# Kernel tuning notes

Measured on AMD Instinct MI355X. Metric: run time of the kernel, lower is better.

## Reference

```python
import jax, jax.numpy as jnp
import numpy as np

N_NODES = 50000
N_EDGES = 800000
HID = 256
OUT = 128
NEG_SLOPE = 0.2


def gat_layer(x, src, dst, W_src, W_dst, a_src_vec, a_dst_vec, bias, n_nodes):
    # Dense projections (PyG lin_src / lin_dst for tuple in_channels)
    h_src = x @ W_src              # [N, C]
    h_dst = x @ W_dst              # [N, C]
    # Per-node attention logits (att_src/att_dst dot products)
    a_src = h_src @ a_src_vec      # [N]
    a_dst = h_dst @ a_dst_vec      # [N]
    # Edge logits + LeakyReLU
    e = jax.nn.leaky_relu(a_src[src] + a_dst[dst], NEG_SLOPE)  # [E]
    # Segment softmax over incoming edges of each dst node
    m = jax.ops.segment_max(e, dst, num_segments=n_nodes)      # [N]
    m = jnp.where(jnp.isfinite(m), m, 0.0)                      # empty segments
    ex = jnp.exp(e - m[dst])                                    # [E]
    s = jax.ops.segment_sum(ex, dst, num_segments=n_nodes)     # [N]
    alpha = ex / (s[dst] + 1e-16)                               # [E]
    # Attention-weighted message aggregation (scatter-add to dst)
    msg = alpha[:, None] * h_src[src]                           # [E, C]
    out = jax.ops.segment_sum(msg, dst, num_segments=n_nodes)  # [N, C]
    return out + bias


def setup_inputs() -> dict:
    key = jax.random.key(0)
    ks = jax.random.split(key, 12)
    x = jax.random.normal(ks[0], (N_NODES, HID), dtype=jnp.float32)
    edge_index = jax.random.randint(ks[1], (2, N_EDGES), 0, N_NODES, dtype=jnp.int64)
    sc1 = 1.0 / np.sqrt(HID)
    sc2 = 1.0 / np.sqrt(HID)
    return {
        "x": x,
        "edge_index": edge_index,
        "W1_src": jax.random.normal(ks[2], (HID, HID), dtype=jnp.float32) * sc1,
        "W1_dst": jax.random.normal(ks[3], (HID, HID), dtype=jnp.float32) * sc1,
        "att1_src": jax.random.normal(ks[4], (HID,), dtype=jnp.float32) * sc1,
        "att1_dst": jax.random.normal(ks[5], (HID,), dtype=jnp.float32) * sc1,
        "b1": jnp.zeros((HID,), dtype=jnp.float32),
        "W2_src": jax.random.normal(ks[6], (HID, OUT), dtype=jnp.float32) * sc2,
        "W2_dst": jax.random.normal(ks[7], (HID, OUT), dtype=jnp.float32) * sc2,
        "att2_src": jax.random.normal(ks[8], (OUT,), dtype=jnp.float32) * (1.0 / np.sqrt(OUT)),
        "att2_dst": jax.random.normal(ks[9], (OUT,), dtype=jnp.float32) * (1.0 / np.sqrt(OUT)),
        "b2": jnp.zeros((OUT,), dtype=jnp.float32),
    }


def reference(x, edge_index, W1_src, W1_dst, att1_src, att1_dst, b1,
              W2_src, W2_dst, att2_src, att2_dst, b2):
    src, dst = edge_index[0], edge_index[1]
    h = gat_layer(x, src, dst, W1_src, W1_dst, att1_src, att1_dst, b1, N_NODES)
    h = jax.nn.relu(h)
    out = gat_layer(h, src, dst, W2_src, W2_dst, att2_src, att2_dst, b2, N_NODES)
    return out
```

## Files before the change

kernel.cpp:

```cpp
#include <hip/hip_runtime.h>
#include <math.h>

#define N_NODES 50000
#define N_EDGES 800000
#define HID 256
#define OUT_C 128
#define NEG_SLOPE 0.2f
#define SCAN_NB ((N_NODES + 255) / 256)

typedef __attribute__((ext_vector_type(8))) short bf16x8;
typedef __attribute__((ext_vector_type(4))) float f32x4;
typedef _Float16 half_t;
typedef __attribute__((ext_vector_type(4))) _Float16 half4;
typedef __attribute__((ext_vector_type(2))) _Float16 half2t;

__device__ inline unsigned short bf16_rne(float x) {
    unsigned u = __float_as_uint(x);
    return (unsigned short)((u + 0x7fffu + ((u >> 16) & 1u)) >> 16);
}


__global__ __launch_bounds__(256) void hist_rank_kernel(
    const int* __restrict__ dst, int* __restrict__ counts, int* __restrict__ rank) {
    int e = blockIdx.x * 256 + threadIdx.x;
    if (e < N_EDGES) rank[e] = atomicAdd(&counts[dst[e]], 1);
}

__global__ __launch_bounds__(256) void block_scan_kernel(
    const int* __restrict__ counts, int* __restrict__ excl,
    int* __restrict__ blockSums, int n) {
    __shared__ int waveSums[4];
    int i = blockIdx.x * 256 + threadIdx.x;
    int lane = threadIdx.x & 63;
    int wv = threadIdx.x >> 6;
    int c = (i < n) ? counts[i] : 0;
    int v = c;
    #pragma unroll
    for (int off = 1; off < 64; off <<= 1) {
        int t = __shfl_up(v, off);
        if (lane >= off) v += t;
    }
    if (lane == 63) waveSums[wv] = v;
    __syncthreads();
    int waveOff = 0;
    #pragma unroll
    for (int w = 0; w < 4; w++)
        if (w < wv) waveOff += waveSums[w];
    if (i < n) excl[i] = waveOff + v - c;
    if (threadIdx.x == 255) blockSums[blockIdx.x] = waveOff + v;
}

__global__ __launch_bounds__(256) void add_offsets_kernel(
    int* __restrict__ excl, const int* __restrict__ blockSums, int n) {
    __shared__ int lds[4];
    int tid = threadIdx.x;
    int partial = 0;
    for (int j = tid; j < (int)blockIdx.x; j += 256) partial += blockSums[j];
    #pragma unroll
    for (int off = 32; off > 0; off >>= 1) partial += __shfl_down(partial, off);
    if ((tid & 63) == 0) lds[tid >> 6] = partial;
    __syncthreads();
    int prefix = lds[0] + lds[1] + lds[2] + lds[3];
    int i = blockIdx.x * 256 + tid;
    if (i < n) excl[i] += prefix;
    if (i == 0) excl[n] = N_EDGES;
}


__global__ __launch_bounds__(256) void edge_weight_kernel(
    const int* __restrict__ src, const int* __restrict__ dst,
    const int* __restrict__ offsets, const int* __restrict__ rank,
    const float* __restrict__ a_src, const float* __restrict__ a_dst,
    int2* __restrict__ ew) {
    int e = blockIdx.x * 256 + threadIdx.x;
    if (e >= N_EDGES) return;
    int s = src[e], d = dst[e];
    float l = a_src[s] + a_dst[d];
    l = fmaxf(l, l * NEG_SLOPE);
    float w = __expf(l);
    ew[offsets[d] + rank[e]] = make_int2(s, __float_as_int(w));
}


__global__ __launch_bounds__(64) void compute_v_all_kernel(
    const float* __restrict__ W1s, const float* __restrict__ att1s,
    const float* __restrict__ W1d, const float* __restrict__ att1d,
    const float* __restrict__ W2s, const float* __restrict__ att2s,
    const float* __restrict__ W2d, const float* __restrict__ att2d,
    float* __restrict__ v1s, float* __restrict__ v1d,
    float* __restrict__ v2s, float* __restrict__ v2d) {
    int k = blockIdx.x;
    int lane = threadIdx.x;
    const float* W; const float* att; float* v; int cout;
    switch (blockIdx.y) {
        case 0: W = W1s; att = att1s; v = v1s; cout = HID; break;
        case 1: W = W1d; att = att1d; v = v1d; cout = HID; break;
        case 2: W = W2s; att = att2s; v = v2s; cout = OUT_C; break;
        default: W = W2d; att = att2d; v = v2d; cout = OUT_C; break;
    }
    float sum = 0.f;
    for (int j = lane; j < cout; j += 64)
        sum += W[k * cout + j] * att[j];
    #pragma unroll
    for (int off = 32; off > 0; off >>= 1)
        sum += __shfl_down(sum, off);
    if (lane == 0) v[k] = sum;
}


#define PACK1_T (8 * 17 * 64)
#define PACK2_T (8 * 9 * 64)

__global__ __launch_bounds__(256) void pack_all_kernel(
    const float* __restrict__ W1, const float* __restrict__ v1s, const float* __restrict__ v1d,
    const float* __restrict__ W2, const float* __restrict__ v2s, const float* __restrict__ v2d,
    unsigned short* __restrict__ hi1, unsigned short* __restrict__ lo1,
    unsigned short* __restrict__ hi2, unsigned short* __restrict__ lo2) {
    int t = blockIdx.x * 256 + threadIdx.x;
    const float *W, *vs, *vd; unsigned short *hi, *lo; int cout, NTL, tt;
    if (t < PACK1_T)            { tt = t;           W = W1; vs = v1s; vd = v1d; hi = hi1; lo = lo1; cout = HID;  NTL = 17; }
    else if (t < PACK1_T + PACK2_T) { tt = t - PACK1_T; W = W2; vs = v2s; vd = v2d; hi = hi2; lo = lo2; cout = OUT_C; NTL = 9; }
    else return;
    int lane = tt & 63;
    int tile = (tt >> 6) % NTL;
    int ks = tt / (64 * NTL);
    int m = lane & 15;
    int kbase = ks * 32 + (lane >> 4) * 8;
    #pragma unroll
    for (int j = 0; j < 8; j++) {
        float val;
        if (tile < NTL - 1) val = W[(kbase + j) * cout + tile * 16 + m];
        else val = (m == 0) ? vs[kbase + j] : (m == 1) ? vd[kbase + j] : 0.f;
        unsigned short h = bf16_rne(val);
        hi[tt * 8 + j] = h;
        lo[tt * 8 + j] = bf16_rne(val - __uint_as_float((unsigned)h << 16));
    }
}


template <int COUT, int NT, bool WRITE_A>
__device__ __forceinline__ void gemm_body(
    const float* __restrict__ A, const unsigned short* __restrict__ Bhi,
    const unsigned short* __restrict__ Blo, half_t* __restrict__ H,
    float* __restrict__ a_s, float* __restrict__ a_d, int M, int tile0) {
    const int NTL = COUT / 16 + 1;
    int wave = threadIdx.x >> 6, lane = threadIdx.x & 63;
    int m = lane & 15, quad = lane >> 4;
    int row0 = blockIdx.x * 128 + wave * 32;
    f32x4 acc[2][NT];
    #pragma unroll
    for (int rg = 0; rg < 2; rg++)
        #pragma unroll
        for (int nt = 0; nt < NT; nt++)
            acc[rg][nt] = (f32x4){0.f, 0.f, 0.f, 0.f};

    const float* arow[2];
    #pragma unroll
    for (int rg = 0; rg < 2; rg++) {
        int r = row0 + rg * 16 + m;
        if (r >= M) r = M - 1;
        arow[rg] = A + (size_t)r * HID;
    }

    for (int ks = 0; ks < 8; ks++) {
        bf16x8 ah[2], al[2];
        #pragma unroll
        for (int rg = 0; rg < 2; rg++) {
            const float* ap = arow[rg] + ks * 32 + quad * 8;
            float4 v0 = *(const float4*)ap;
            float4 v1 = *(const float4*)(ap + 4);
            float av[8] = {v0.x, v0.y, v0.z, v0.w, v1.x, v1.y, v1.z, v1.w};
            #pragma unroll
            for (int j = 0; j < 8; j++) {
                unsigned short h = bf16_rne(av[j]);
                float hf = __uint_as_float((unsigned)h << 16);
                ah[rg][j] = (short)h;
                al[rg][j] = (short)bf16_rne(av[j] - hf);
            }
        }
        #pragma unroll
        for (int nt = 0; nt < NT; nt++) {
            int tile = (WRITE_A && nt == NT - 1) ? (COUT / 16) : (tile0 + nt);
            size_t fbase = ((size_t)(ks * NTL + tile) * 64 + lane) * 8;
            bf16x8 bh = *(const bf16x8*)(Bhi + fbase);
            bf16x8 bl = *(const bf16x8*)(Blo + fbase);
            acc[0][nt] = __builtin_amdgcn_mfma_f32_16x16x32_bf16(ah[0], bh, acc[0][nt], 0, 0, 0);
            acc[1][nt] = __builtin_amdgcn_mfma_f32_16x16x32_bf16(ah[1], bh, acc[1][nt], 0, 0, 0);
            acc[0][nt] = __builtin_amdgcn_mfma_f32_16x16x32_bf16(ah[0], bl, acc[0][nt], 0, 0, 0);
            acc[1][nt] = __builtin_amdgcn_mfma_f32_16x16x32_bf16(ah[1], bl, acc[1][nt], 0, 0, 0);
            acc[0][nt] = __builtin_amdgcn_mfma_f32_16x16x32_bf16(al[0], bh, acc[0][nt], 0, 0, 0);
            acc[1][nt] = __builtin_amdgcn_mfma_f32_16x16x32_bf16(al[1], bh, acc[1][nt], 0, 0, 0);
        }
    }
    const int NW = WRITE_A ? NT - 1 : NT;
    #pragma unroll
    for (int rg = 0; rg < 2; rg++)
        #pragma unroll
        for (int nt = 0; nt < NW; nt++)
            #pragma unroll
            for (int r = 0; r < 4; r++) {
                int row = row0 + rg * 16 + quad * 4 + r;
                if (row < M)
                    H[(size_t)row * COUT + (tile0 + nt) * 16 + m] = (half_t)acc[rg][nt][r];
            }
    if (WRITE_A) {
        #pragma unroll
        for (int rg = 0; rg < 2; rg++)
            #pragma unroll
            for (int r = 0; r < 4; r++) {
                int row = row0 + rg * 16 + quad * 4 + r;
                if (row < M) {
                    if (m == 0) a_s[row] = acc[rg][NT - 1][r];
                    else if (m == 1) a_d[row] = acc[rg][NT - 1][r];
                }
            }
    }
}

template <int COUT>
__global__ __launch_bounds__(256) void mfma_gemm_a_kernel(
    const float* __restrict__ A, const unsigned short* __restrict__ Bhi,
    const unsigned short* __restrict__ Blo, half_t* __restrict__ H,
    float* __restrict__ a_s, float* __restrict__ a_d, int M) {
    if (blockIdx.y == 0)
        gemm_body<COUT, 9, true>(A, Bhi, Blo, H, a_s, a_d, M, 0);
    else
        gemm_body<COUT, 8, false>(A, Bhi, Blo, H, a_s, a_d, M, 8);
}


template <int C, bool RELU>
__global__ __launch_bounds__(256) void fused_aggregate_kernel(
    const int* __restrict__ offsets, const int2* __restrict__ ew,
    const half_t* __restrict__ h, const float* __restrict__ bias,
    float* __restrict__ out) {
    constexpr int CH = 8;
    int node = (int)((blockIdx.x * 256u + threadIdx.x) >> 6);
    int lane = threadIdx.x & 63;
    if (node >= N_NODES) return;
    int beg = offsets[node], end = offsets[node + 1];
    float s = 0.f;

    if (C == 256) {
        float4 acc = make_float4(0.f, 0.f, 0.f, 0.f);
        for (int base = beg; base < end; base += CH) {
            int cnt = end - base; if (cnt > CH) cnt = CH;
            int2 e[CH];
            #pragma unroll
            for (int j = 0; j < CH; j++)
                e[j] = ew[(j < cnt) ? base + j : base];
            half4 hv[CH];
            #pragma unroll
            for (int j = 0; j < CH; j++)
                hv[j] = *(const half4*)(h + ((unsigned)e[j].x * C + lane * 4));
            #pragma unroll
            for (int j = 0; j < CH; j++) {
                float w = (j < cnt) ? __int_as_float(e[j].y) : 0.f;
                s += w;
                acc.x += w * (float)hv[j][0]; acc.y += w * (float)hv[j][1];
                acc.z += w * (float)hv[j][2]; acc.w += w * (float)hv[j][3];
            }
        }
        float inv = 1.f / (s + 1e-16f);
        float4 bv = *(const float4*)(bias + lane * 4);
        acc.x = acc.x * inv + bv.x; acc.y = acc.y * inv + bv.y;
        acc.z = acc.z * inv + bv.z; acc.w = acc.w * inv + bv.w;
        if (RELU) {
            acc.x = fmaxf(acc.x, 0.f); acc.y = fmaxf(acc.y, 0.f);
            acc.z = fmaxf(acc.z, 0.f); acc.w = fmaxf(acc.w, 0.f);
        }
        *(float4*)(out + (size_t)node * C + lane * 4) = acc;
    } else {
        float2 acc = make_float2(0.f, 0.f);
        for (int base = beg; base < end; base += CH) {
            int cnt = end - base; if (cnt > CH) cnt = CH;
            int2 e[CH];
            #pragma unroll
            for (int j = 0; j < CH; j++)
                e[j] = ew[(j < cnt) ? base + j : base];
            half2t hv[CH];
            #pragma unroll
            for (int j = 0; j < CH; j++)
                hv[j] = *(const half2t*)(h + ((unsigned)e[j].x * C + lane * 2));
            #pragma unroll
            for (int j = 0; j < CH; j++) {
                float w = (j < cnt) ? __int_as_float(e[j].y) : 0.f;
                s += w;
                acc.x += w * (float)hv[j][0]; acc.y += w * (float)hv[j][1];
            }
        }
        float inv = 1.f / (s + 1e-16f);
        float2 bv = *(const float2*)(bias + lane * 2);
        acc.x = acc.x * inv + bv.x; acc.y = acc.y * inv + bv.y;
        if (RELU) { acc.x = fmaxf(acc.x, 0.f); acc.y = fmaxf(acc.y, 0.f); }
        *(float2*)(out + (size_t)node * C + lane * 2) = acc;
    }
}

extern "C" void kernel_launch(void* const* d_in, const int* in_sizes, int n_in,
                              void* d_out, int out_size, void* d_ws, size_t ws_size,
                              hipStream_t stream) {
    const float* x     = (const float*)d_in[0];
    const int*   edge  = (const int*)d_in[1];
    const int*   src   = edge;
    const int*   dst   = edge + N_EDGES;
    const float* W1s   = (const float*)d_in[2];
    const float* W1d   = (const float*)d_in[3];
    const float* att1s = (const float*)d_in[4];
    const float* att1d = (const float*)d_in[5];
    const float* b1    = (const float*)d_in[6];
    const float* W2s   = (const float*)d_in[7];
    const float* W2d   = (const float*)d_in[8];
    const float* att2s = (const float*)d_in[9];
    const float* att2d = (const float*)d_in[10];
    const float* b2    = (const float*)d_in[11];
    float* out = (float*)d_out;

    float* ws    = (float*)d_ws;
    half_t* h1   = (half_t*)ws;
    int2* ew     = (int2*)(ws + (size_t)N_NODES * HID / 2);
    float* act2  = ws + (size_t)N_NODES * HID;
    float* a_s   = act2 + (size_t)N_NODES * HID;
    float* a_d   = a_s + N_NODES;
    float* vbuf  = a_d + N_NODES;
    int* ibase      = (int*)(vbuf + 4 * HID);
    int* rank       = ibase;
    int* counts     = rank + N_EDGES;
    int* offsets    = counts + N_NODES;
    int* blockSums  = offsets + N_NODES + 1;
    unsigned short* wp1h = (unsigned short*)(((uintptr_t)(blockSums + SCAN_NB) + 15) & ~(uintptr_t)15);
    unsigned short* wp1l = wp1h + PACK1_T * 8;
    unsigned short* wp2h = wp1l + PACK1_T * 8;
    unsigned short* wp2l = wp2h + PACK2_T * 8;
    float* v1s = vbuf, *v1d = vbuf + HID, *v2s = vbuf + 2 * HID, *v2d = vbuf + 3 * HID;
    half_t* h2 = h1;

    const int edgeBlocks = (N_EDGES + 255) / 256;
    const int waveBlocksN = (N_NODES + 3) / 4;
    const int gemmBlocks = (N_NODES + 127) / 128;

    hipMemsetAsync(counts, 0, N_NODES * sizeof(int), stream);
    hist_rank_kernel<<<edgeBlocks, 256, 0, stream>>>(dst, counts, rank);
    block_scan_kernel<<<SCAN_NB, 256, 0, stream>>>(counts, offsets, blockSums, N_NODES);
    add_offsets_kernel<<<SCAN_NB, 256, 0, stream>>>(offsets, blockSums, N_NODES);

    compute_v_all_kernel<<<dim3(HID, 4), 64, 0, stream>>>(
        W1s, att1s, W1d, att1d, W2s, att2s, W2d, att2d, v1s, v1d, v2s, v2d);
    pack_all_kernel<<<(PACK1_T + PACK2_T + 255) / 256, 256, 0, stream>>>(
        W1s, v1s, v1d, W2s, v2s, v2d, wp1h, wp1l, wp2h, wp2l);

    mfma_gemm_a_kernel<HID><<<dim3(gemmBlocks, 2), 256, 0, stream>>>(
        x, wp1h, wp1l, h1, a_s, a_d, N_NODES);
    edge_weight_kernel<<<edgeBlocks, 256, 0, stream>>>(
        src, dst, offsets, rank, a_s, a_d, ew);
    fused_aggregate_kernel<HID, true><<<waveBlocksN, 256, 0, stream>>>(
        offsets, ew, h1, b1, act2);

    mfma_gemm_a_kernel<OUT_C><<<dim3(gemmBlocks, 1), 256, 0, stream>>>(
        act2, wp2h, wp2l, h2, a_s, a_d, N_NODES);
    edge_weight_kernel<<<edgeBlocks, 256, 0, stream>>>(
        src, dst, offsets, rank, a_s, a_d, ew);
    fused_aggregate_kernel<OUT_C, false><<<waveBlocksN, 256, 0, stream>>>(
        offsets, ew, h2, b2, out);
}
```

Baseline: 361.9 us.

## Pack multiple nodes per wave in aggregation with 16-byte gathers and shuffled edge loads

The aggregation kernel now assigns 2 nodes (C=256) or 4 nodes (C=128) per 64-lane wave, so each lane handles 8 channels and gathers a 16-byte half8 vector per edge. Edge records are loaded cooperatively, one per lane, and broadcast with width-limited shuffles instead of every lane reloading all of them. The chunk size rises to 16 edges. The goal is fewer wasted lanes and wider memory transactions for the low-degree (about 16 edges) gather, in exchange for more registers and shuffle overhead.

```diff
diff --git a/kernel.cpp b/kernel.cpp
--- a/kernel.cpp
+++ b/kernel.cpp
@@ -11,8 +11,7 @@
 typedef __attribute__((ext_vector_type(8))) short bf16x8;
 typedef __attribute__((ext_vector_type(4))) float f32x4;
 typedef _Float16 half_t;
-typedef __attribute__((ext_vector_type(4))) _Float16 half4;
-typedef __attribute__((ext_vector_type(2))) _Float16 half2t;
+typedef __attribute__((ext_vector_type(8))) _Float16 half8;
 
 __device__ inline unsigned short bf16_rne(float x) {
     unsigned u = __float_as_uint(x);
@@ -234,67 +233,62 @@
     const int* __restrict__ offsets, const int2* __restrict__ ew,
     const half_t* __restrict__ h, const float* __restrict__ bias,
     float* __restrict__ out) {
-    constexpr int CH = 8;
-    int node = (int)((blockIdx.x * 256u + threadIdx.x) >> 6);
+    constexpr int CH = 16;
+    constexpr int G = (C == 256) ? 32 : 16;
+    constexpr int NPW = 64 / G;
+    int wid = blockIdx.x * 4 + (threadIdx.x >> 6);
     int lane = threadIdx.x & 63;
+    int sub = lane / G;
+    int gl = lane & (G - 1);
+    int node = wid * NPW + sub;
     if (node >= N_NODES) return;
     int beg = offsets[node], end = offsets[node + 1];
-    float s = 0.f;
-
-    if (C == 256) {
-        float4 acc = make_float4(0.f, 0.f, 0.f, 0.f);
-        for (int base = beg; base < end; base += CH) {
-            int cnt = end - base; if (cnt > CH) cnt = CH;
-            int2 e[CH];
+    float ssum = 0.f;
+    float acc[8];
+    #pragma unroll
+    for (int k = 0; k < 8; k++) acc[k] = 0.f;
+    unsigned c0 = (unsigned)gl * 8u;
+
+    for (int base = beg; base < end; base += CH) {
+        int cnt = end - base; if (cnt > CH) cnt = CH;
+        int li = gl & (CH - 1);
+        int eidx = base + ((li < cnt) ? li : 0);
+        int2 ev = ew[eidx];
+        int idxs[CH]; float w[CH];
+        #pragma unroll
+        for (int j = 0; j < CH; j++) {
+            idxs[j] = __shfl(ev.x, j, G);
+            float wv = __int_as_float(__shfl(ev.y, j, G));
+            w[j] = (j < cnt) ? wv : 0.f;
+        }
+        half8 hv[CH];
+        #pragma unroll
+        for (int j = 0; j < CH; j++)
+            hv[j] = *(const half8*)(h + ((size_t)(unsigned)idxs[j] * C + c0));
+        #pragma unroll
+        for (int j = 0; j < CH; j++) {
+            ssum += w[j];
             #pragma unroll
-            for (int j = 0; j < CH; j++)
-                e[j] = ew[(j < cnt) ? base + j : base];
-            half4 hv[CH];
-            #pragma unroll
-            for (int j = 0; j < CH; j++)
-                hv[j] = *(const half4*)(h + ((unsigned)e[j].x * C + lane * 4));
-            #pragma unroll
-            for (int j = 0; j < CH; j++) {
-                float w = (j < cnt) ? __int_as_float(e[j].y) : 0.f;
-                s += w;
-                acc.x += w * (float)hv[j][0]; acc.y += w * (float)hv[j][1];
-                acc.z += w * (float)hv[j][2]; acc.w += w * (float)hv[j][3];
-            }
+            for (int k = 0; k < 8; k++)
+                acc[k] += w[j] * (float)hv[j][k];
         }
-        float inv = 1.f / (s + 1e-16f);
-        float4 bv = *(const float4*)(bias + lane * 4);
-        acc.x = acc.x * inv + bv.x; acc.y = acc.y * inv + bv.y;
-        acc.z = acc.z * inv + bv.z; acc.w = acc.w * inv + bv.w;
-        if (RELU) {
-            acc.x = fmaxf(acc.x, 0.f); acc.y = fmaxf(acc.y, 0.f);
-            acc.z = fmaxf(acc.z, 0.f); acc.w = fmaxf(acc.w, 0.f);
-        }
-        *(float4*)(out + (size_t)node * C + lane * 4) = acc;
-    } else {
-        float2 acc = make_float2(0.f, 0.f);
-        for (int base = beg; base < end; base += CH) {
-            int cnt = end - base; if (cnt > CH) cnt = CH;
-            int2 e[CH];
-            #pragma unroll
-            for (int j = 0; j < CH; j++)
-                e[j] = ew[(j < cnt) ? base + j : base];
-            half2t hv[CH];
-            #pragma unroll
-            for (int j = 0; j < CH; j++)
-                hv[j] = *(const half2t*)(h + ((unsigned)e[j].x * C + lane * 2));
-            #pragma unroll
-            for (int j = 0; j < CH; j++) {
-                float w = (j < cnt) ? __int_as_float(e[j].y) : 0.f;
-                s += w;
-                acc.x += w * (float)hv[j][0]; acc.y += w * (float)hv[j][1];
-            }
-        }
-        float inv = 1.f / (s + 1e-16f);
-        float2 bv = *(const float2*)(bias + lane * 2);
-        acc.x = acc.x * inv + bv.x; acc.y = acc.y * inv + bv.y;
-        if (RELU) { acc.x = fmaxf(acc.x, 0.f); acc.y = fmaxf(acc.y, 0.f); }
-        *(float2*)(out + (size_t)node * C + lane * 2) = acc;
-    }
+    }
+
+    float inv = 1.f / (ssum + 1e-16f);
+    float4 bv0 = *(const float4*)(bias + c0);
+    float4 bv1 = *(const float4*)(bias + c0 + 4);
+    float o[8];
+    o[0] = acc[0] * inv + bv0.x; o[1] = acc[1] * inv + bv0.y;
+    o[2] = acc[2] * inv + bv0.z; o[3] = acc[3] * inv + bv0.w;
+    o[4] = acc[4] * inv + bv1.x; o[5] = acc[5] * inv + bv1.y;
+    o[6] = acc[6] * inv + bv1.z; o[7] = acc[7] * inv + bv1.w;
+    if (RELU) {
+        #pragma unroll
+        for (int k = 0; k < 8; k++) o[k] = fmaxf(o[k], 0.f);
+    }
+    float* op = out + (size_t)node * C + c0;
+    *(float4*)op       = make_float4(o[0], o[1], o[2], o[3]);
+    *(float4*)(op + 4) = make_float4(o[4], o[5], o[6], o[7]);
 }
 
 extern "C" void kernel_launch(void* const* d_in, const int* in_sizes, int n_in,
@@ -336,8 +330,9 @@
     half_t* h2 = h1;
 
     const int edgeBlocks = (N_EDGES + 255) / 256;
-    const int waveBlocksN = (N_NODES + 3) / 4;
     const int gemmBlocks = (N_NODES + 127) / 128;
+    const int aggBlocks1 = ((N_NODES + 1) / 2 + 3) / 4;
+    const int aggBlocks2 = ((N_NODES + 3) / 4 + 3) / 4;
 
     hipMemsetAsync(counts, 0, N_NODES * sizeof(int), stream);
     hist_rank_kernel<<<edgeBlocks, 256, 0, stream>>>(dst, counts, rank);
@@ -353,13 +348,13 @@
         x, wp1h, wp1l, h1, a_s, a_d, N_NODES);
     edge_weight_kernel<<<edgeBlocks, 256, 0, stream>>>(
         src, dst, offsets, rank, a_s, a_d, ew);
-    fused_aggregate_kernel<HID, true><<<waveBlocksN, 256, 0, stream>>>(
+    fused_aggregate_kernel<HID, true><<<aggBlocks1, 256, 0, stream>>>(
         offsets, ew, h1, b1, act2);
 
     mfma_gemm_a_kernel<OUT_C><<<dim3(gemmBlocks, 1), 256, 0, stream>>>(
         act2, wp2h, wp2l, h2, a_s, a_d, N_NODES);
     edge_weight_kernel<<<edgeBlocks, 256, 0, stream>>>(
         src, dst, offsets, rank, a_s, a_d, ew);
-    fused_aggregate_kernel<OUT_C, false><<<waveBlocksN, 256, 0, stream>>>(
+    fused_aggregate_kernel<OUT_C, false><<<aggBlocks2, 256, 0, stream>>>(
         offsets, ew, h2, b2, out);
 }
```

Result: no change. 364.4 us (+0.7%).
